# Optimization experiments

Hardware: AMD Instinct MI355X
Metric: run time of the kernel (lower is better)

Reference implementation:

```python
import jax, jax.numpy as jnp
import numpy as np

B, L, S, D, H = 2, 2048, 2048, 256, 8
HD = D // H  # per-head dim = 32
EPS = 1e-5


def _layernorm(x, g, b):
    m = jnp.mean(x, axis=-1, keepdims=True)
    v = jnp.mean(jnp.square(x - m), axis=-1, keepdims=True)
    return (x - m) * jax.lax.rsqrt(v + EPS) * g + b


def setup_inputs() -> dict:
    key = jax.random.key(0)
    ks = jax.random.split(key, 12)
    w = lambda k, o, i: jax.random.normal(k, (o, i), dtype=jnp.float32) * (1.0 / np.sqrt(i))
    return {
        "x": jax.random.normal(ks[0], (B, L, D), dtype=jnp.float32),
        "source": jax.random.normal(ks[1], (B, S, D), dtype=jnp.float32),
        "attn_factor": jax.random.uniform(ks[2], (B, L, S), dtype=jnp.float32),
        "Wq": w(ks[3], D, D),
        "Wk": w(ks[4], D, D),
        "Wv": w(ks[5], D, D),
        "Wm": w(ks[6], D, D),
        "W1": w(ks[7], 2 * D, 2 * D),
        "W2": w(ks[8], D, 2 * D),
        "g1": jnp.ones((D,), jnp.float32),
        "b1": jnp.zeros((D,), jnp.float32),
        "g2": jnp.ones((D,), jnp.float32),
        "b2": jnp.zeros((D,), jnp.float32),
    }


def reference(x, source, attn_factor, Wq, Wk, Wv, Wm, W1, W2, g1, b1, g2, b2):
    bs, l, d = x.shape
    s = source.shape[1]
    # projections (torch Linear: y = x @ W^T), split heads
    qw = (x @ Wq.T).reshape(bs, l, H, HD)       # [B,L,H,hd]
    kw = (source @ Wk.T).reshape(bs, s, H, HD)  # [B,S,H,hd]
    vw = (source @ Wv.T).reshape(bs, s, H, HD)  # [B,S,H,hd]
    # QK^T -> [B,L,S,H], scale, elementwise attn_factor, softmax over S
    a = jnp.einsum("nlhd,nshd->nlsh", qw, kw)
    a = a / np.sqrt(HD)
    a = a * attn_factor[:, :, :, None]
    a = jax.nn.softmax(a, axis=2)
    # AV -> [B,L,H,hd] -> merge heads
    o = jnp.einsum("nlsh,nshd->nlhd", a, vw).reshape(bs, l, d)
    message = o @ Wm.T
    message = _layernorm(message, g1, b1)
    h = jnp.concatenate([x, message], axis=2)       # [B,L,2D]
    h = jnp.maximum(h @ W1.T, 0.0)                  # ReLU MLP
    message = h @ W2.T                              # [B,L,D]
    message = _layernorm(message, g2, b2)
    return x + message
```

## Files before the change

kernel.cpp:

```cpp
#include <hip/hip_runtime.h>
#include <hip/hip_bf16.h>
#include <math.h>

#define B_  2
#define L_  2048
#define S_  2048
#define D_  256
#define H_  8
#define HD_ 32
#define ML_ (B_ * L_)
#define MS_ (B_ * S_)
#define NSPLIT 4
#define SCHUNK (S_ / NSPLIT)

typedef __attribute__((ext_vector_type(8))) short short8;
typedef __attribute__((ext_vector_type(4))) float f32x4;

__global__ __launch_bounds__(256) void convert_all(
    const float* __restrict__ x,  const float* __restrict__ src,
    const float* __restrict__ Wq, const float* __restrict__ Wk,
    const float* __restrict__ Wv, const float* __restrict__ Wm,
    const float* __restrict__ W1, const float* __restrict__ W2,
    __hip_bfloat16* xb,  __hip_bfloat16* srcb,
    __hip_bfloat16* Wqb, __hip_bfloat16* Wkb,
    __hip_bfloat16* Wvb, __hip_bfloat16* Wmb,
    __hip_bfloat16* W1b, __hip_bfloat16* W2b) {
    const size_t i4 = ((size_t)blockIdx.x * 256 + threadIdx.x) * 4;
    const float* sp; __hip_bfloat16* dp; size_t off;
    if      (i4 < 1048576) { sp = x;   dp = xb;   off = i4; }
    else if (i4 < 2097152) { sp = src; dp = srcb; off = i4 - 1048576; }
    else if (i4 < 2162688) { sp = Wq;  dp = Wqb;  off = i4 - 2097152; }
    else if (i4 < 2228224) { sp = Wk;  dp = Wkb;  off = i4 - 2162688; }
    else if (i4 < 2293760) { sp = Wv;  dp = Wvb;  off = i4 - 2228224; }
    else if (i4 < 2359296) { sp = Wm;  dp = Wmb;  off = i4 - 2293760; }
    else if (i4 < 2621440) { sp = W1;  dp = W1b;  off = i4 - 2359296; }
    else                   { sp = W2;  dp = W2b;  off = i4 - 2621440; }
    float4 v = *(const float4*)(sp + off);
    __hip_bfloat16 o0 = __float2bfloat16(v.x), o1 = __float2bfloat16(v.y);
    __hip_bfloat16 o2 = __float2bfloat16(v.z), o3 = __float2bfloat16(v.w);
    __hip_bfloat16* d = dp + off;
    d[0] = o0; d[1] = o1; d[2] = o2; d[3] = o3;
}

template <bool RELU, typename OutT>
__device__ __forceinline__ void gemm_body(const __hip_bfloat16* __restrict__ A,
                                          const __hip_bfloat16* __restrict__ A2,
                                          const __hip_bfloat16* __restrict__ Bm,
                                          OutT* __restrict__ C,
                                          int N, int K, int lda, int m0, int n0,
                                          float cscale,
                                          __hip_bfloat16 (&As)[64][72],
                                          __hip_bfloat16 (&Bs)[64][72]) {
    const int tid  = threadIdx.x;
    const int w    = tid >> 6;
    const int lane = tid & 63;
    const int colL = lane & 15;
    const int quad = lane >> 4;
    const int mh = (w & 1) * 32, nh = (w >> 1) * 32;
    const int srow = tid >> 3;
    const int scg  = (tid & 7) * 8;

    f32x4 acc[2][2] = {};

    auto loadA = [&](int p, int k0) -> short8 {
        const __hip_bfloat16* Asrc = A; int kk = k0;
        if (A2 && k0 >= 256) { Asrc = A2; kk = k0 - 256; }
        return *(const short8*)(Asrc + (size_t)(m0 + srow + p * 32) * lda + kk + scg);
    };
    auto loadB = [&](int p, int k0) -> short8 {
        return *(const short8*)(Bm + (size_t)(n0 + srow + p * 32) * K + k0 + scg);
    };

    short8 ra[2], rb[2];
#pragma unroll
    for (int p = 0; p < 2; ++p) { ra[p] = loadA(p, 0); rb[p] = loadB(p, 0); }

    for (int k0 = 0; k0 < K; k0 += 64) {
        __syncthreads();
#pragma unroll
        for (int p = 0; p < 2; ++p) {
            *(short8*)&As[srow + p * 32][scg] = ra[p];
            *(short8*)&Bs[srow + p * 32][scg] = rb[p];
        }
        __syncthreads();
        if (k0 + 64 < K) {
#pragma unroll
            for (int p = 0; p < 2; ++p) { ra[p] = loadA(p, k0 + 64); rb[p] = loadB(p, k0 + 64); }
        }
#pragma unroll
        for (int ks = 0; ks < 2; ++ks) {
            short8 af[2], bf[2];
#pragma unroll
            for (int i = 0; i < 2; ++i)
                af[i] = *(const short8*)&As[mh + i * 16 + colL][ks * 32 + quad * 8];
#pragma unroll
            for (int j = 0; j < 2; ++j)
                bf[j] = *(const short8*)&Bs[nh + j * 16 + colL][ks * 32 + quad * 8];
#pragma unroll
            for (int i = 0; i < 2; ++i)
#pragma unroll
                for (int j = 0; j < 2; ++j)
                    acc[i][j] = __builtin_amdgcn_mfma_f32_16x16x32_bf16(af[i], bf[j], acc[i][j], 0, 0, 0);
        }
    }
#pragma unroll
    for (int i = 0; i < 2; ++i)
#pragma unroll
        for (int r = 0; r < 4; ++r) {
            const size_t row = m0 + mh + i * 16 + quad * 4 + r;
#pragma unroll
            for (int j = 0; j < 2; ++j) {
                float v = acc[i][j][r] * cscale;
                if (RELU) v = fmaxf(v, 0.f);
                C[row * N + n0 + nh + j * 16 + colL] = (OutT)v;
            }
        }
}

template <bool RELU, typename OutT>
__global__ __launch_bounds__(256) void gemm_bf16(const __hip_bfloat16* __restrict__ A,
                                                 const __hip_bfloat16* __restrict__ A2,
                                                 const __hip_bfloat16* __restrict__ Bm,
                                                 OutT* __restrict__ C,
                                                 int N, int K, int lda) {
    __shared__ __hip_bfloat16 As[64][72];
    __shared__ __hip_bfloat16 Bs[64][72];
    gemm_body<RELU, OutT>(A, A2, Bm, C, N, K, lda,
                          blockIdx.x * 64, blockIdx.y * 64, 1.f, As, Bs);
}

__global__ __launch_bounds__(256) void proj_fused(const __hip_bfloat16* __restrict__ x_b,
                                                  const __hip_bfloat16* __restrict__ src_b,
                                                  const __hip_bfloat16* __restrict__ Wq_b,
                                                  const __hip_bfloat16* __restrict__ Wk_b,
                                                  const __hip_bfloat16* __restrict__ Wv_b,
                                                  __hip_bfloat16* __restrict__ Qb,
                                                  __hip_bfloat16* __restrict__ Kb,
                                                  __hip_bfloat16* __restrict__ Vtb) {
    __shared__ __hip_bfloat16 As[64][72];
    __shared__ __hip_bfloat16 Bs[64][72];
    const int id = blockIdx.x;
    if (id < 256) {
        gemm_body<false, __hip_bfloat16>(x_b, nullptr, Wq_b, Qb, 256, 256, 256,
                                         (id >> 2) * 64, (id & 3) * 64,
                                         0.17677669529663687f, As, Bs);
    } else if (id < 512) {
        const int t = id - 256;
        gemm_body<false, __hip_bfloat16>(src_b, nullptr, Wk_b, Kb, 256, 256, 256,
                                         (t >> 2) * 64, (t & 3) * 64, 1.f, As, Bs);
    } else {
        const int t = id - 512;
        const int b = t >> 7, u = t & 127;
        gemm_body<false, __hip_bfloat16>(Wv_b, nullptr, src_b + (size_t)b * S_ * D_,
                                         Vtb + (size_t)b * D_ * S_, S_, 256, 256,
                                         (u & 3) * 64, (u >> 2) * 64, 1.f, As, Bs);
    }
}

__global__ __launch_bounds__(256, 4) void attn_mfma(const __hip_bfloat16* __restrict__ Qb,
                                                    const __hip_bfloat16* __restrict__ Kb,
                                                    const __hip_bfloat16* __restrict__ Vtb,
                                                    const float* __restrict__ F,
                                                    __hip_bfloat16* __restrict__ Op,
                                                    float* __restrict__ Ll) {
    const int tid  = threadIdx.x;
    const int w    = tid >> 6;
    const int lane = tid & 63;
    const int colL = lane & 15;
    const int quad = lane >> 4;

    const int b     = blockIdx.z >> 2;
    const int split = blockIdx.z & 3;
    const int h     = blockIdx.y;
    const int qw    = blockIdx.x * 64 + w * 16;

    __shared__ __hip_bfloat16 Ks[64][40];
    __shared__ __hip_bfloat16 Vs[32][72];
    __shared__ __hip_bfloat16 Pw[4][16][72];

    const short8 aq = *(const short8*)(Qb + ((size_t)(b * L_ + qw + colL)) * D_ + h * HD_ + quad * 8);

    float lsum[4] = {0.f, 0.f, 0.f, 0.f};
    f32x4 o0 = {0.f, 0.f, 0.f, 0.f}, o1 = {0.f, 0.f, 0.f, 0.f};

    const int kr = tid >> 2, kc = (tid & 3) * 8;
    const int vr = tid >> 3, vc = (tid & 7) * 8;
    const __hip_bfloat16* kst = Kb + ((size_t)(b * S_ + kr)) * D_ + h * HD_ + kc;
    const __hip_bfloat16* vst = Vtb + (size_t)b * D_ * S_ + ((size_t)(h * HD_ + vr)) * S_ + vc;
    const float* fbase = F + ((size_t)(b * L_ + qw + quad * 4)) * S_ + colL;

    const int sbeg = split * SCHUNK, send = sbeg + SCHUNK;
    short8 rk = *(const short8*)(kst + (size_t)sbeg * D_);
    short8 rv = *(const short8*)(vst + sbeg);

    for (int s0 = sbeg; s0 < send; s0 += 64) {
        __syncthreads();
        *(short8*)&Ks[kr][kc] = rk;
        *(short8*)&Vs[vr][vc] = rv;
        __syncthreads();
        if (s0 + 64 < send) {
            rk = *(const short8*)(kst + (size_t)(s0 + 64) * D_);
            rv = *(const short8*)(vst + s0 + 64);
        }
        f32x4 cc[4];
#pragma unroll
        for (int n = 0; n < 4; ++n) {
            short8 kf = *(const short8*)&Ks[n * 16 + colL][quad * 8];
            f32x4 z = {0.f, 0.f, 0.f, 0.f};
            cc[n] = __builtin_amdgcn_mfma_f32_16x16x32_bf16(aq, kf, z, 0, 0, 0);
        }
#pragma unroll
        for (int n = 0; n < 4; ++n)
#pragma unroll
            for (int r = 0; r < 4; ++r) {
                float fv = fbase[(size_t)r * S_ + s0 + n * 16];
                float p = __expf(cc[n][r] * fv);
                lsum[r] += p;
                Pw[w][quad * 4 + r][n * 16 + colL] = __float2bfloat16(p);
            }
        short8 a0 = *(const short8*)(&Pw[w][colL][quad * 8]);
        short8 a1 = *(const short8*)(&Pw[w][colL][32 + quad * 8]);
#pragma unroll
        for (int ks = 0; ks < 2; ++ks) {
            short8 ap = ks ? a1 : a0;
#pragma unroll
            for (int nt = 0; nt < 2; ++nt) {
                short8 vf = *(const short8*)&Vs[nt * 16 + colL][ks * 32 + quad * 8];
                if (nt == 0) o0 = __builtin_amdgcn_mfma_f32_16x16x32_bf16(ap, vf, o0, 0, 0, 0);
                else         o1 = __builtin_amdgcn_mfma_f32_16x16x32_bf16(ap, vf, o1, 0, 0, 0);
            }
        }
    }

#pragma unroll
    for (int r = 0; r < 4; ++r) {
        float t = lsum[r];
        t += __shfl_xor(t, 1);
        t += __shfl_xor(t, 2);
        t += __shfl_xor(t, 4);
        t += __shfl_xor(t, 8);
        lsum[r] = t;
    }

#pragma unroll
    for (int r = 0; r < 4; ++r) {
        const size_t row = (size_t)(b * L_ + qw + quad * 4 + r);
        const size_t po = ((size_t)split * ML_ + row) * D_ + h * HD_;
        Op[po + colL]      = __float2bfloat16(o0[r]);
        Op[po + 16 + colL] = __float2bfloat16(o1[r]);
        if (colL == 0)
            Ll[((size_t)split * H_ + h) * ML_ + row] = lsum[r];
    }
}

__global__ __launch_bounds__(256) void attn_combine(const __hip_bfloat16* __restrict__ Op,
                                                    const float* __restrict__ Ll,
                                                    __hip_bfloat16* __restrict__ o_b) {
    const int idx = blockIdx.x * 256 + threadIdx.x;
    const int row = idx >> 8, d = idx & 255, h = d >> 5;
    float Lt = 0.f, acc = 0.f;
#pragma unroll
    for (int s = 0; s < NSPLIT; ++s) {
        Lt  += Ll[((size_t)s * H_ + h) * ML_ + row];
        acc += __bfloat162float(Op[((size_t)s * ML_ + row) * D_ + d]);
    }
    o_b[idx] = __float2bfloat16(acc / Lt);
}

template <typename OutT>
__global__ __launch_bounds__(256) void gemm_ln(const __hip_bfloat16* __restrict__ A,
                                               const __hip_bfloat16* __restrict__ Bm,
                                               const float* __restrict__ g,
                                               const float* __restrict__ bb,
                                               const float* __restrict__ resid,
                                               OutT* __restrict__ Y,
                                               int K) {
    __shared__ __hip_bfloat16 As[16][72];
    __shared__ __hip_bfloat16 Bs[256][72];
    __shared__ float gs[256], bs_[256];
    __shared__ float stats[4][16][2];
    const int tid  = threadIdx.x;
    const int w    = tid >> 6;
    const int lane = tid & 63;
    const int colL = lane & 15;
    const int quad = lane >> 4;
    const int nh = w * 64;
    const int m0 = blockIdx.x * 16;
    const int srow = tid >> 3;
    const int scg  = (tid & 7) * 8;

    gs[tid] = g[tid]; bs_[tid] = bb[tid];

    f32x4 acc[4] = {};

    auto loadA = [&](int k0) -> short8 {
        return *(const short8*)(A + (size_t)(m0 + srow) * K + k0 + scg);
    };
    auto loadB = [&](int p, int k0) -> short8 {
        return *(const short8*)(Bm + (size_t)(srow + p * 32) * K + k0 + scg);
    };

    short8 ra = {};
    if (srow < 16) ra = loadA(0);
    short8 rb[8];
#pragma unroll
    for (int p = 0; p < 8; ++p) rb[p] = loadB(p, 0);

    for (int k0 = 0; k0 < K; k0 += 64) {
        __syncthreads();
        if (srow < 16) *(short8*)&As[srow][scg] = ra;
#pragma unroll
        for (int p = 0; p < 8; ++p)
            *(short8*)&Bs[srow + p * 32][scg] = rb[p];
        __syncthreads();
        if (k0 + 64 < K) {
            if (srow < 16) ra = loadA(k0 + 64);
#pragma unroll
            for (int p = 0; p < 8; ++p) rb[p] = loadB(p, k0 + 64);
        }
#pragma unroll
        for (int ks = 0; ks < 2; ++ks) {
            short8 af = *(const short8*)&As[colL][ks * 32 + quad * 8];
#pragma unroll
            for (int j = 0; j < 4; ++j) {
                short8 bf = *(const short8*)&Bs[nh + j * 16 + colL][ks * 32 + quad * 8];
                acc[j] = __builtin_amdgcn_mfma_f32_16x16x32_bf16(af, bf, acc[j], 0, 0, 0);
            }
        }
    }

#pragma unroll
    for (int r = 0; r < 4; ++r) {
        float s = 0.f, q = 0.f;
#pragma unroll
        for (int j = 0; j < 4; ++j) {
            float v = acc[j][r];
            s += v; q += v * v;
        }
        s += __shfl_xor(s, 1); q += __shfl_xor(q, 1);
        s += __shfl_xor(s, 2); q += __shfl_xor(q, 2);
        s += __shfl_xor(s, 4); q += __shfl_xor(q, 4);
        s += __shfl_xor(s, 8); q += __shfl_xor(q, 8);
        if (colL == 0) {
            stats[w][quad * 4 + r][0] = s;
            stats[w][quad * 4 + r][1] = q;
        }
    }
    __syncthreads();

#pragma unroll
    for (int r = 0; r < 4; ++r) {
        const int row = quad * 4 + r;
        const float S = stats[0][row][0] + stats[1][row][0] + stats[2][row][0] + stats[3][row][0];
        const float Q = stats[0][row][1] + stats[1][row][1] + stats[2][row][1] + stats[3][row][1];
        const float mean = S * (1.f / 256.f);
        const float var  = Q * (1.f / 256.f) - mean * mean;
        const float rstd = rsqrtf(var + 1e-5f);
        const size_t grow = (size_t)(m0 + row) * 256;
#pragma unroll
        for (int j = 0; j < 4; ++j) {
            const int col = nh + j * 16 + colL;
            float y = (acc[j][r] - mean) * rstd * gs[col] + bs_[col];
            if (resid) y += resid[grow + col];
            Y[grow + col] = (OutT)y;
        }
    }
}

extern "C" void kernel_launch(void* const* d_in, const int* in_sizes, int n_in,
                              void* d_out, int out_size, void* d_ws, size_t ws_size,
                              hipStream_t stream) {
    (void)in_sizes; (void)n_in; (void)out_size; (void)ws_size;
    const float* x   = (const float*)d_in[0];
    const float* src = (const float*)d_in[1];
    const float* F   = (const float*)d_in[2];
    const float* Wq  = (const float*)d_in[3];
    const float* Wk  = (const float*)d_in[4];
    const float* Wv  = (const float*)d_in[5];
    const float* Wm  = (const float*)d_in[6];
    const float* W1  = (const float*)d_in[7];
    const float* W2  = (const float*)d_in[8];
    const float* g1  = (const float*)d_in[9];
    const float* b1  = (const float*)d_in[10];
    const float* g2  = (const float*)d_in[11];
    const float* b2  = (const float*)d_in[12];
    float* out = (float*)d_out;

    char* ws = (char*)d_ws;
    __hip_bfloat16* x_b   = (__hip_bfloat16*)(ws);
    __hip_bfloat16* src_b = (__hip_bfloat16*)(ws + (2u << 20));
    __hip_bfloat16* Wq_b  = (__hip_bfloat16*)(ws + (4u << 20));
    __hip_bfloat16* Wk_b  = (__hip_bfloat16*)(ws + (4u << 20) + 131072);
    __hip_bfloat16* Wv_b  = (__hip_bfloat16*)(ws + (4u << 20) + 2 * 131072);
    __hip_bfloat16* Wm_b  = (__hip_bfloat16*)(ws + (4u << 20) + 3 * 131072);
    __hip_bfloat16* W1_b  = (__hip_bfloat16*)(ws + (4u << 20) + 4 * 131072);
    __hip_bfloat16* W2_b  = (__hip_bfloat16*)(ws + (4u << 20) + 4 * 131072 + 524288);
    __hip_bfloat16* Qb   = (__hip_bfloat16*)(ws + (6u << 20));
    __hip_bfloat16* Kb   = (__hip_bfloat16*)(ws + (8u << 20));
    __hip_bfloat16* Vtb  = (__hip_bfloat16*)(ws + (10u << 20));
    __hip_bfloat16* o_b  = (__hip_bfloat16*)(ws + (12u << 20));
    __hip_bfloat16* Opart = (__hip_bfloat16*)(ws + (14u << 20));
    float* Ll  = (float*)(ws + (22u << 20));
    __hip_bfloat16* m1_b = (__hip_bfloat16*)(ws + (18u << 20));
    __hip_bfloat16* h_b  = (__hip_bfloat16*)(ws + (20u << 20));

    dim3 blk(256);
    convert_all<<<dim3(2688), blk, 0, stream>>>(x, src, Wq, Wk, Wv, Wm, W1, W2,
                                                x_b, src_b, Wq_b, Wk_b, Wv_b, Wm_b, W1_b, W2_b);
    proj_fused<<<dim3(1024), blk, 0, stream>>>(x_b, src_b, Wq_b, Wk_b, Wv_b, Qb, Kb, Vtb);
    attn_mfma<<<dim3(L_ / 64, H_, B_ * NSPLIT), blk, 0, stream>>>(Qb, Kb, Vtb, F, Opart, Ll);
    attn_combine<<<dim3(ML_ * D_ / 256), blk, 0, stream>>>(Opart, Ll, o_b);
    gemm_ln<__hip_bfloat16><<<dim3(ML_ / 16), blk, 0, stream>>>(o_b, Wm_b, g1, b1, nullptr, m1_b, 256);
    gemm_bf16<true, __hip_bfloat16><<<dim3(ML_ / 64, 512 / 64), blk, 0, stream>>>(x_b, m1_b, W1_b, h_b, 512, 512, 256);
    gemm_ln<float><<<dim3(ML_ / 16), blk, 0, stream>>>(h_b, W2_b, g2, b2, x, out, 512);
}
```

Baseline: 167.3 us.

## Fuse split-attention combine into Wm GEMM+LayerNorm and widen attention K/V tiles

```diff
diff --git a/kernel.cpp b/kernel.cpp
--- a/kernel.cpp
+++ b/kernel.cpp
@@ -174,8 +174,8 @@
     const int h     = blockIdx.y;
     const int qw    = blockIdx.x * 64 + w * 16;
 
-    __shared__ __hip_bfloat16 Ks[64][40];
-    __shared__ __hip_bfloat16 Vs[32][72];
+    __shared__ __hip_bfloat16 Ks[128][40];
+    __shared__ __hip_bfloat16 Vs[32][136];
     __shared__ __hip_bfloat16 Pw[4][16][72];
 
     const short8 aq = *(const short8*)(Qb + ((size_t)(b * L_ + qw + colL)) * D_ + h * HD_ + quad * 8);
@@ -190,44 +190,57 @@
     const float* fbase = F + ((size_t)(b * L_ + qw + quad * 4)) * S_ + colL;
 
     const int sbeg = split * SCHUNK, send = sbeg + SCHUNK;
-    short8 rk = *(const short8*)(kst + (size_t)sbeg * D_);
-    short8 rv = *(const short8*)(vst + sbeg);
-
-    for (int s0 = sbeg; s0 < send; s0 += 64) {
-        __syncthreads();
-        *(short8*)&Ks[kr][kc] = rk;
-        *(short8*)&Vs[vr][vc] = rv;
-        __syncthreads();
-        if (s0 + 64 < send) {
-            rk = *(const short8*)(kst + (size_t)(s0 + 64) * D_);
-            rv = *(const short8*)(vst + s0 + 64);
-        }
-        f32x4 cc[4];
-#pragma unroll
-        for (int n = 0; n < 4; ++n) {
-            short8 kf = *(const short8*)&Ks[n * 16 + colL][quad * 8];
-            f32x4 z = {0.f, 0.f, 0.f, 0.f};
-            cc[n] = __builtin_amdgcn_mfma_f32_16x16x32_bf16(aq, kf, z, 0, 0, 0);
-        }
-#pragma unroll
-        for (int n = 0; n < 4; ++n)
-#pragma unroll
-            for (int r = 0; r < 4; ++r) {
-                float fv = fbase[(size_t)r * S_ + s0 + n * 16];
-                float p = __expf(cc[n][r] * fv);
-                lsum[r] += p;
-                Pw[w][quad * 4 + r][n * 16 + colL] = __float2bfloat16(p);
-            }
-        short8 a0 = *(const short8*)(&Pw[w][colL][quad * 8]);
-        short8 a1 = *(const short8*)(&Pw[w][colL][32 + quad * 8]);
-#pragma unroll
-        for (int ks = 0; ks < 2; ++ks) {
-            short8 ap = ks ? a1 : a0;
-#pragma unroll
-            for (int nt = 0; nt < 2; ++nt) {
-                short8 vf = *(const short8*)&Vs[nt * 16 + colL][ks * 32 + quad * 8];
-                if (nt == 0) o0 = __builtin_amdgcn_mfma_f32_16x16x32_bf16(ap, vf, o0, 0, 0, 0);
-                else         o1 = __builtin_amdgcn_mfma_f32_16x16x32_bf16(ap, vf, o1, 0, 0, 0);
+    short8 rk[2], rv[2];
+#pragma unroll
+    for (int p = 0; p < 2; ++p) {
+        rk[p] = *(const short8*)(kst + (size_t)(sbeg + p * 64) * D_);
+        rv[p] = *(const short8*)(vst + sbeg + p * 64);
+    }
+
+    for (int s0 = sbeg; s0 < send; s0 += 128) {
+        __syncthreads();
+        *(short8*)&Ks[kr][kc]        = rk[0];
+        *(short8*)&Ks[kr + 64][kc]   = rk[1];
+        *(short8*)&Vs[vr][vc]        = rv[0];
+        *(short8*)&Vs[vr][vc + 64]   = rv[1];
+        __syncthreads();
+        if (s0 + 128 < send) {
+#pragma unroll
+            for (int p = 0; p < 2; ++p) {
+                rk[p] = *(const short8*)(kst + (size_t)(s0 + 128 + p * 64) * D_);
+                rv[p] = *(const short8*)(vst + s0 + 128 + p * 64);
+            }
+        }
+#pragma unroll
+        for (int hs = 0; hs < 2; ++hs) {
+            const int sh = s0 + hs * 64;
+            f32x4 cc[4];
+#pragma unroll
+            for (int n = 0; n < 4; ++n) {
+                short8 kf = *(const short8*)&Ks[hs * 64 + n * 16 + colL][quad * 8];
+                f32x4 z = {0.f, 0.f, 0.f, 0.f};
+                cc[n] = __builtin_amdgcn_mfma_f32_16x16x32_bf16(aq, kf, z, 0, 0, 0);
+            }
+#pragma unroll
+            for (int n = 0; n < 4; ++n)
+#pragma unroll
+                for (int r = 0; r < 4; ++r) {
+                    float fv = fbase[(size_t)r * S_ + sh + n * 16];
+                    float p = __expf(cc[n][r] * fv);
+                    lsum[r] += p;
+                    Pw[w][quad * 4 + r][n * 16 + colL] = __float2bfloat16(p);
+                }
+            short8 a0 = *(const short8*)(&Pw[w][colL][quad * 8]);
+            short8 a1 = *(const short8*)(&Pw[w][colL][32 + quad * 8]);
+#pragma unroll
+            for (int ks = 0; ks < 2; ++ks) {
+                short8 ap = ks ? a1 : a0;
+#pragma unroll
+                for (int nt = 0; nt < 2; ++nt) {
+                    short8 vf = *(const short8*)&Vs[nt * 16 + colL][hs * 64 + ks * 32 + quad * 8];
+                    if (nt == 0) o0 = __builtin_amdgcn_mfma_f32_16x16x32_bf16(ap, vf, o0, 0, 0, 0);
+                    else         o1 = __builtin_amdgcn_mfma_f32_16x16x32_bf16(ap, vf, o1, 0, 0, 0);
+                }
             }
         }
     }
@@ -253,18 +266,129 @@
     }
 }
 
-__global__ __launch_bounds__(256) void attn_combine(const __hip_bfloat16* __restrict__ Op,
-                                                    const float* __restrict__ Ll,
-                                                    __hip_bfloat16* __restrict__ o_b) {
-    const int idx = blockIdx.x * 256 + threadIdx.x;
-    const int row = idx >> 8, d = idx & 255, h = d >> 5;
-    float Lt = 0.f, acc = 0.f;
-#pragma unroll
-    for (int s = 0; s < NSPLIT; ++s) {
-        Lt  += Ll[((size_t)s * H_ + h) * ML_ + row];
-        acc += __bfloat162float(Op[((size_t)s * ML_ + row) * D_ + d]);
-    }
-    o_b[idx] = __float2bfloat16(acc / Lt);
+__global__ __launch_bounds__(256) void gemm_ln_att(const __hip_bfloat16* __restrict__ Opart,
+                                                   const float* __restrict__ Ll,
+                                                   const __hip_bfloat16* __restrict__ Bm,
+                                                   const float* __restrict__ g,
+                                                   const float* __restrict__ bb,
+                                                   __hip_bfloat16* __restrict__ Y) {
+    __shared__ __hip_bfloat16 As[16][72];
+    __shared__ __hip_bfloat16 Bs[256][72];
+    __shared__ float gs[256], bs_[256];
+    __shared__ float stats[4][16][2];
+    __shared__ float Linv[16][8];
+    const int tid  = threadIdx.x;
+    const int w    = tid >> 6;
+    const int lane = tid & 63;
+    const int colL = lane & 15;
+    const int quad = lane >> 4;
+    const int nh = w * 64;
+    const int m0 = blockIdx.x * 16;
+    const int srow = tid >> 3;
+    const int scg  = (tid & 7) * 8;
+    const int K = 256;
+
+    gs[tid] = g[tid]; bs_[tid] = bb[tid];
+    if (tid < 128) {
+        const int row = tid >> 3, hh = tid & 7;
+        float t = 0.f;
+#pragma unroll
+        for (int s = 0; s < NSPLIT; ++s)
+            t += Ll[((size_t)s * H_ + hh) * ML_ + m0 + row];
+        Linv[row][hh] = 1.f / t;
+    }
+    __syncthreads();
+
+    f32x4 acc[4] = {};
+
+    auto loadA = [&](int k0) -> short8 {
+        const float inv = Linv[srow][(k0 + scg) >> 5];
+        float a[8] = {};
+#pragma unroll
+        for (int s = 0; s < NSPLIT; ++s) {
+            short8 v = *(const short8*)(Opart + ((size_t)s * ML_ + m0 + srow) * 256 + k0 + scg);
+#pragma unroll
+            for (int e = 0; e < 8; ++e) {
+                union { short s16; __hip_bfloat16 h; } c; c.s16 = v[e];
+                a[e] += __bfloat162float(c.h);
+            }
+        }
+        short8 outv;
+#pragma unroll
+        for (int e = 0; e < 8; ++e) {
+            union { __hip_bfloat16 h; short s16; } c;
+            c.h = __float2bfloat16(a[e] * inv);
+            outv[e] = c.s16;
+        }
+        return outv;
+    };
+    auto loadB = [&](int p, int k0) -> short8 {
+        return *(const short8*)(Bm + (size_t)(srow + p * 32) * K + k0 + scg);
+    };
+
+    short8 ra = {};
+    if (srow < 16) ra = loadA(0);
+    short8 rb[8];
+#pragma unroll
+    for (int p = 0; p < 8; ++p) rb[p] = loadB(p, 0);
+
+    for (int k0 = 0; k0 < K; k0 += 64) {
+        __syncthreads();
+        if (srow < 16) *(short8*)&As[srow][scg] = ra;
+#pragma unroll
+        for (int p = 0; p < 8; ++p)
+            *(short8*)&Bs[srow + p * 32][scg] = rb[p];
+        __syncthreads();
+        if (k0 + 64 < K) {
+            if (srow < 16) ra = loadA(k0 + 64);
+#pragma unroll
+            for (int p = 0; p < 8; ++p) rb[p] = loadB(p, k0 + 64);
+        }
+#pragma unroll
+        for (int ks = 0; ks < 2; ++ks) {
+            short8 af = *(const short8*)&As[colL][ks * 32 + quad * 8];
+#pragma unroll
+            for (int j = 0; j < 4; ++j) {
+                short8 bf = *(const short8*)&Bs[nh + j * 16 + colL][ks * 32 + quad * 8];
+                acc[j] = __builtin_amdgcn_mfma_f32_16x16x32_bf16(af, bf, acc[j], 0, 0, 0);
+            }
+        }
+    }
+
+#pragma unroll
+    for (int r = 0; r < 4; ++r) {
+        float s = 0.f, q = 0.f;
+#pragma unroll
+        for (int j = 0; j < 4; ++j) {
+            float v = acc[j][r];
+            s += v; q += v * v;
+        }
+        s += __shfl_xor(s, 1); q += __shfl_xor(q, 1);
+        s += __shfl_xor(s, 2); q += __shfl_xor(q, 2);
+        s += __shfl_xor(s, 4); q += __shfl_xor(q, 4);
+        s += __shfl_xor(s, 8); q += __shfl_xor(q, 8);
+        if (colL == 0) {
+            stats[w][quad * 4 + r][0] = s;
+            stats[w][quad * 4 + r][1] = q;
+        }
+    }
+    __syncthreads();
+
+#pragma unroll
+    for (int r = 0; r < 4; ++r) {
+        const int row = quad * 4 + r;
+        const float S = stats[0][row][0] + stats[1][row][0] + stats[2][row][0] + stats[3][row][0];
+        const float Q = stats[0][row][1] + stats[1][row][1] + stats[2][row][1] + stats[3][row][1];
+        const float mean = S * (1.f / 256.f);
+        const float var  = Q * (1.f / 256.f) - mean * mean;
+        const float rstd = rsqrtf(var + 1e-5f);
+        const size_t grow = (size_t)(m0 + row) * 256;
+#pragma unroll
+        for (int j = 0; j < 4; ++j) {
+            const int col = nh + j * 16 + colL;
+            Y[grow + col] = __float2bfloat16((acc[j][r] - mean) * rstd * gs[col] + bs_[col]);
+        }
+    }
 }
 
 template <typename OutT>
@@ -398,10 +522,9 @@
     __hip_bfloat16* Qb   = (__hip_bfloat16*)(ws + (6u << 20));
     __hip_bfloat16* Kb   = (__hip_bfloat16*)(ws + (8u << 20));
     __hip_bfloat16* Vtb  = (__hip_bfloat16*)(ws + (10u << 20));
-    __hip_bfloat16* o_b  = (__hip_bfloat16*)(ws + (12u << 20));
+    __hip_bfloat16* m1_b = (__hip_bfloat16*)(ws + (12u << 20));
     __hip_bfloat16* Opart = (__hip_bfloat16*)(ws + (14u << 20));
     float* Ll  = (float*)(ws + (22u << 20));
-    __hip_bfloat16* m1_b = (__hip_bfloat16*)(ws + (18u << 20));
     __hip_bfloat16* h_b  = (__hip_bfloat16*)(ws + (20u << 20));
 
     dim3 blk(256);
@@ -409,8 +532,7 @@
                                                 x_b, src_b, Wq_b, Wk_b, Wv_b, Wm_b, W1_b, W2_b);
     proj_fused<<<dim3(1024), blk, 0, stream>>>(x_b, src_b, Wq_b, Wk_b, Wv_b, Qb, Kb, Vtb);
     attn_mfma<<<dim3(L_ / 64, H_, B_ * NSPLIT), blk, 0, stream>>>(Qb, Kb, Vtb, F, Opart, Ll);
-    attn_combine<<<dim3(ML_ * D_ / 256), blk, 0, stream>>>(Opart, Ll, o_b);
-    gemm_ln<__hip_bfloat16><<<dim3(ML_ / 16), blk, 0, stream>>>(o_b, Wm_b, g1, b1, nullptr, m1_b, 256);
+    gemm_ln_att<<<dim3(ML_ / 16), blk, 0, stream>>>(Opart, Ll, Wm_b, g1, b1, m1_b);
     gemm_bf16<true, __hip_bfloat16><<<dim3(ML_ / 64, 512 / 64), blk, 0, stream>>>(x_b, m1_b, W1_b, h_b, 512, 512, 256);
     gemm_ln<float><<<dim3(ML_ / 16), blk, 0, stream>>>(h_b, W2_b, g2, b2, x, out, 512);
 }
```

After: 164.2 us. Within noise of the previous version (-1.9%).
